# Kernel optimization log

Measured on AMD Instinct MI355X. Metric: run time of the kernel, lower is better.

Reference implementation:

```python
import jax, jax.numpy as jnp
import numpy as np

B, S, D = 1, 4096, 512
H, DK, DV = 8, 64, 64


def setup_inputs() -> dict:
    key = jax.random.key(0)
    ks = jax.random.split(key, 8)
    s = 1.0 / np.sqrt(D)
    return {
        "queries": jax.random.normal(ks[0], (B, S, D), jnp.float32),
        "keys": jax.random.normal(ks[1], (B, S, D), jnp.float32),
        "values": jax.random.normal(ks[2], (B, S, D), jnp.float32),
        # Linear weights stored as [in, out] for x @ W
        "Wq": jax.random.normal(ks[3], (D, H * DK), jnp.float32) * s,
        "Wk": jax.random.normal(ks[4], (D, H * DK), jnp.float32) * s,
        "Wv": jax.random.normal(ks[5], (D, H * DV), jnp.float32) * s,
        "Wo": jax.random.normal(ks[6], (H * DV, D), jnp.float32) * s,
        "bo": jax.random.normal(ks[7], (D,), jnp.float32) * 0.02,
    }


def reference(queries, keys, values, Wq, Wk, Wv, Wo, bo):
    b, qlen = values.shape[0], queries.shape[1]
    q = (queries @ Wq).reshape(b, qlen, H, DK)
    k = (keys @ Wk).reshape(b, keys.shape[1], H, DK)
    v = (values @ Wv).reshape(b, values.shape[1], H, DV)
    scale = DK ** 0.5
    # naive full attention: materialize [b, h, sq, sk] scores
    scores = jnp.einsum("bqhd,bkhd->bhqk", q, k) / scale
    attn = jax.nn.softmax(scores, axis=-1)
    out = jnp.einsum("bhqk,bkhd->bqhd", attn, v).reshape(b, qlen, H * DV)
    out = out @ Wo + bo          # first fc_out
    out = out @ Wo + bo          # second fc_out (module applies it twice when not reversible)
    return out
```

## Files before the change

kernel.cpp:

```cpp
#include <hip/hip_runtime.h>

#define S_LEN  4096
#define DMODEL 512
#define NH     8
#define HD     64

typedef _Float16 f16x8 __attribute__((ext_vector_type(8)));
typedef _Float16 f16x4 __attribute__((ext_vector_type(4)));
typedef float    f32x4 __attribute__((ext_vector_type(4)));

static __device__ __forceinline__ unsigned short f2h(float x) {
  return __builtin_bit_cast(unsigned short, (_Float16)x);
}

__global__ __launch_bounds__(256) void wtrans_kernel(
    const float* __restrict__ w0, const float* __restrict__ w1,
    const float* __restrict__ w2, const float* __restrict__ w3,
    unsigned short* __restrict__ o0, unsigned short* __restrict__ o1,
    unsigned short* __restrict__ o2, unsigned short* __restrict__ o3,
    unsigned short* __restrict__ o3s)
{
  __shared__ unsigned short T[64 * 72];
  const float* W; unsigned short* O;
  switch (blockIdx.z) {
    case 0:  W = w0; O = o0; break;
    case 1:  W = w1; O = o1; break;
    case 2:  W = w2; O = o2; break;
    default: W = w3; O = o3; break;
  }
  const int tid = threadIdx.x;
  const int k0 = blockIdx.x * 64, n0 = blockIdx.y * 64;
  const int c4 = (tid & 15) * 4;
#pragma unroll
  for (int rp = 0; rp < 4; ++rp) {
    int r = rp * 16 + (tid >> 4);
    float4 x = *(const float4*)(W + (k0 + r) * DMODEL + n0 + c4);
    T[(c4 + 0) * 72 + r] = f2h(x.x);
    T[(c4 + 1) * 72 + r] = f2h(x.y);
    T[(c4 + 2) * 72 + r] = f2h(x.z);
    T[(c4 + 3) * 72 + r] = f2h(x.w);
    if (blockIdx.z == 3) {
      f16x4 st;
      st[0] = (_Float16)x.x; st[1] = (_Float16)x.y;
      st[2] = (_Float16)x.z; st[3] = (_Float16)x.w;
      *(f16x4*)&o3s[(k0 + r) * DMODEL + n0 + c4] = st;
    }
  }
  __syncthreads();
#pragma unroll
  for (int it = 0; it < 2; ++it) {
    int i = tid + it * 256;
    int nl = i >> 3, c = i & 7;
    *(f16x8*)&O[(n0 + nl) * DMODEL + k0 + c * 8] = *(const f16x8*)&T[nl * 72 + c * 8];
  }
}

__global__ __launch_bounds__(256) void gemm_kernel(
    const void* __restrict__ A0, const void* __restrict__ A1,
    const void* __restrict__ A2, const void* __restrict__ A3,
    const unsigned short* __restrict__ B0, const unsigned short* __restrict__ B1,
    const unsigned short* __restrict__ B2, const unsigned short* __restrict__ B3,
    void* __restrict__ C0, void* __restrict__ C1,
    void* __restrict__ C2, void* __restrict__ C3,
    const float* __restrict__ bias, unsigned short* __restrict__ vtg,
    const float* __restrict__ wo_f32, const float* __restrict__ bo_in,
    float* __restrict__ bo2_out,
    int a_fp32_mask, int c_fp32_mask)
{
  constexpr int K = DMODEL, N = DMODEL;
  __shared__ unsigned short As[64 * 32];
  __shared__ unsigned short Bs[64 * 32];
  const int z = blockIdx.z;
  if (z == 3 && blockIdx.x >= 8) {
    if (blockIdx.x < 16 && blockIdx.y == 0 && wo_f32) {
      int col = (blockIdx.x - 8) * 64 + (threadIdx.x & 63);
      float s = bo_in[col];
#pragma unroll 8
      for (int j = 0; j < DMODEL; ++j) s = fmaf(bo_in[j], wo_f32[j * DMODEL + col], s);
      bo2_out[col] = s;
    }
    return;
  }
  const void* Av; const unsigned short* Bt; void* Cv;
  switch (z) {
    case 0:  Av = A0; Bt = B0; Cv = C0; break;
    case 1:  Av = A1; Bt = B1; Cv = C1; break;
    case 2:  Av = A2; Bt = B2; Cv = C2; break;
    default: Av = A3; Bt = B3; Cv = C3; break;
  }
  const int a_fp32 = (a_fp32_mask >> z) & 1;
  const int c_fp32 = (c_fp32_mask >> z) & 1;
  const int tid  = threadIdx.x;
  const int lane = tid & 63;
  const int wid  = tid >> 6;
  const int quad = lane >> 4, l16 = lane & 15;
  const int m0 = blockIdx.x * 64, n0 = blockIdx.y * 64;
  const int wm = (wid >> 1) * 32, wn = (wid & 1) * 32;
  const int r  = tid >> 2, ck = (tid & 3) * 8;
  f32x4 acc[2][2] = {};

  for (int k0 = 0; k0 < K; k0 += 32) {
    __syncthreads();
    if (a_fp32) {
      const float* p = (const float*)Av + (m0 + r) * K + k0 + ck;
      float4 x = *(const float4*)p;
      float4 y = *(const float4*)(p + 4);
      f16x8 av;
      av[0] = (_Float16)x.x; av[1] = (_Float16)x.y;
      av[2] = (_Float16)x.z; av[3] = (_Float16)x.w;
      av[4] = (_Float16)y.x; av[5] = (_Float16)y.y;
      av[6] = (_Float16)y.z; av[7] = (_Float16)y.w;
      *(f16x8*)&As[r * 32 + ck] = av;
    } else {
      *(f16x8*)&As[r * 32 + ck] =
          *(const f16x8*)((const unsigned short*)Av + (m0 + r) * K + k0 + ck);
    }
    *(f16x8*)&Bs[r * 32 + ck] = *(const f16x8*)(Bt + (n0 + r) * K + k0 + ck);
    __syncthreads();

    f16x8 a0 = *(const f16x8*)&As[(wm + l16) * 32 + quad * 8];
    f16x8 a1 = *(const f16x8*)&As[(wm + 16 + l16) * 32 + quad * 8];
    f16x8 b0 = *(const f16x8*)&Bs[(wn + l16) * 32 + quad * 8];
    f16x8 b1 = *(const f16x8*)&Bs[(wn + 16 + l16) * 32 + quad * 8];
    acc[0][0] = __builtin_amdgcn_mfma_f32_16x16x32_f16(a0, b0, acc[0][0], 0, 0, 0);
    acc[0][1] = __builtin_amdgcn_mfma_f32_16x16x32_f16(a0, b1, acc[0][1], 0, 0, 0);
    acc[1][0] = __builtin_amdgcn_mfma_f32_16x16x32_f16(a1, b0, acc[1][0], 0, 0, 0);
    acc[1][1] = __builtin_amdgcn_mfma_f32_16x16x32_f16(a1, b1, acc[1][1], 0, 0, 0);
  }

  const int do_vt = (vtg != nullptr) && (z == 2);
#pragma unroll
  for (int mt = 0; mt < 2; ++mt)
#pragma unroll
    for (int nt = 0; nt < 2; ++nt) {
      int col = n0 + wn + nt * 16 + l16;
      float bv = bias ? bias[col] : 0.f;
#pragma unroll
      for (int g = 0; g < 4; ++g) {
        int row = m0 + wm + mt * 16 + quad * 4 + g;
        float val = acc[mt][nt][g] + bv;
        if (do_vt)        vtg[col * S_LEN + row] = f2h(val);
        else if (c_fp32)  ((float*)Cv)[row * N + col] = val;
        else              ((unsigned short*)Cv)[row * N + col] = f2h(val);
      }
    }
}

__global__ __launch_bounds__(256) void attn_kernel(
    const unsigned short* __restrict__ Qb, const unsigned short* __restrict__ Kb,
    const unsigned short* __restrict__ VtG, unsigned short* __restrict__ Ob)
{
  __shared__ unsigned short Ks[2][64 * 72];
  __shared__ unsigned short Vt[2][64 * 72];
  __shared__ _Float16 Osc[2][64][32];
  __shared__ float    Msc[2][2][16];
  __shared__ float    Lsc[2][2][16];

  const int tid  = threadIdx.x;
  const int lane = tid & 63;
  const int wid  = tid >> 6;
  const int qp   = wid & 1;
  const int kh   = wid >> 1;
  const int quad = lane >> 4, l16 = lane & 15;
  const int qb = blockIdx.x, h = blockIdx.y;
  const int hc = h * HD;
  const int qbase = qb * 64 + qp * 32;

  f16x8 bq[2][2];
#pragma unroll
  for (int s = 0; s < 2; ++s) {
    int qrow = qbase + s * 16 + l16;
    bq[s][0] = *(const f16x8*)(Qb + qrow * DMODEL + hc + quad * 8);
    bq[s][1] = *(const f16x8*)(Qb + qrow * DMODEL + hc + 32 + quad * 8);
  }

  f32x4 o[2][4] = {};
  float m_run[2] = {-1e30f, -1e30f}, l_run[2] = {0.f, 0.f};

  f16x8 kreg[4], vreg[4];
#pragma unroll
  for (int it = 0; it < 4; ++it) {
    int s = it * 256 + tid;
    int khs = s >> 9, n = (s >> 3) & 63, c = s & 7;
    kreg[it] = *(const f16x8*)(Kb + (khs * 2048 + n) * DMODEL + hc + c * 8);
    vreg[it] = *(const f16x8*)(VtG + (hc + n) * S_LEN + khs * 2048 + c * 8);
  }

  for (int kbi = 0; kbi < 32; ++kbi) {
    __syncthreads();
#pragma unroll
    for (int it = 0; it < 4; ++it) {
      int s = it * 256 + tid;
      int khs = s >> 9, n = (s >> 3) & 63, c = s & 7;
      *(f16x8*)&Ks[khs][n * 72 + c * 8] = kreg[it];
      *(f16x8*)&Vt[khs][n * 72 + c * 8] = vreg[it];
    }
    __syncthreads();

    if (kbi + 1 < 32) {
      int kb1 = (kbi + 1) * 64;
#pragma unroll
      for (int it = 0; it < 4; ++it) {
        int s = it * 256 + tid;
        int khs = s >> 9, n = (s >> 3) & 63, c = s & 7;
        kreg[it] = *(const f16x8*)(Kb + (khs * 2048 + kb1 + n) * DMODEL + hc + c * 8);
        vreg[it] = *(const f16x8*)(VtG + (hc + n) * S_LEN + khs * 2048 + kb1 + c * 8);
      }
    }

    f32x4 sT[2][4];
#pragma unroll
    for (int kt = 0; kt < 4; ++kt) {
      f16x8 ak0 = *(const f16x8*)&Ks[kh][(kt * 16 + l16) * 72 + quad * 8];
      f16x8 ak1 = *(const f16x8*)&Ks[kh][(kt * 16 + l16) * 72 + 32 + quad * 8];
#pragma unroll
      for (int s = 0; s < 2; ++s) {
        f32x4 a = {};
        a = __builtin_amdgcn_mfma_f32_16x16x32_f16(ak0, bq[s][0], a, 0, 0, 0);
        a = __builtin_amdgcn_mfma_f32_16x16x32_f16(ak1, bq[s][1], a, 0, 0, 0);
        sT[s][kt] = a;
      }
    }

    f16x4 pa[2][4];
#pragma unroll
    for (int s = 0; s < 2; ++s) {
      float vmax = -1e30f;
#pragma unroll
      for (int kt = 0; kt < 4; ++kt)
#pragma unroll
        for (int g = 0; g < 4; ++g) vmax = fmaxf(vmax, sT[s][kt][g]);
      vmax = fmaxf(vmax, __shfl_xor(vmax, 16));
      vmax = fmaxf(vmax, __shfl_xor(vmax, 32));
      const float mn = fmaxf(m_run[s], vmax);
      const float alpha = __expf((m_run[s] - mn) * 0.125f);
      m_run[s] = mn;

      float rs = 0.f;
#pragma unroll
      for (int kt = 0; kt < 4; ++kt)
#pragma unroll
        for (int g = 0; g < 4; ++g) {
          float p = __expf((sT[s][kt][g] - mn) * 0.125f);
          rs += p;
          pa[s][kt][g] = (_Float16)p;
        }
      rs += __shfl_xor(rs, 16);
      rs += __shfl_xor(rs, 32);
      l_run[s] = l_run[s] * alpha + rs;

      float ag[4];
#pragma unroll
      for (int g = 0; g < 4; ++g) ag[g] = __shfl(alpha, quad * 4 + g);
#pragma unroll
      for (int nt = 0; nt < 4; ++nt)
#pragma unroll
        for (int g = 0; g < 4; ++g) o[s][nt][g] *= ag[g];
    }

#pragma unroll
    for (int nt = 0; nt < 4; ++nt)
#pragma unroll
      for (int kt = 0; kt < 4; ++kt) {
        f16x4 bv = *(const f16x4*)&Vt[kh][(nt * 16 + l16) * 72 + kt * 16 + quad * 4];
#pragma unroll
        for (int s = 0; s < 2; ++s)
          o[s][nt] = __builtin_amdgcn_mfma_f32_16x16x16f16(pa[s][kt], bv, o[s][nt], 0, 0, 0);
      }
  }

  __syncthreads();
  if (kh == 1) {
#pragma unroll
    for (int s = 0; s < 2; ++s) {
      if (quad == 0) { Msc[qp][s][l16] = m_run[s]; Lsc[qp][s][l16] = l_run[s]; }
#pragma unroll
      for (int nt = 0; nt < 4; ++nt)
#pragma unroll
        for (int g = 0; g < 4; ++g)
          Osc[qp][lane][s * 16 + nt * 4 + g] = (_Float16)o[s][nt][g];
    }
  }
  __syncthreads();
  if (kh == 0) {
#pragma unroll
    for (int s = 0; s < 2; ++s) {
      const float m1 = Msc[qp][s][l16];
      const float l1 = Lsc[qp][s][l16];
      const float m  = fmaxf(m_run[s], m1);
      const float a0 = __expf((m_run[s] - m) * 0.125f);
      const float a1 = __expf((m1 - m) * 0.125f);
      const float rl = 1.f / (l_run[s] * a0 + l1 * a1);
      float a0g[4], a1g[4], rlg[4];
#pragma unroll
      for (int g = 0; g < 4; ++g) {
        a0g[g] = __shfl(a0, quad * 4 + g);
        a1g[g] = __shfl(a1, quad * 4 + g);
        rlg[g] = __shfl(rl, quad * 4 + g);
      }
#pragma unroll
      for (int g = 0; g < 4; ++g) {
        int row = qbase + s * 16 + quad * 4 + g;
#pragma unroll
        for (int nt = 0; nt < 4; ++nt) {
          float om = o[s][nt][g] * a0g[g] + (float)Osc[qp][lane][s * 16 + nt * 4 + g] * a1g[g];
          Ob[row * DMODEL + hc + nt * 16 + l16] = f2h(om * rlg[g]);
        }
      }
    }
  }
}

extern "C" void kernel_launch(void* const* d_in, const int* in_sizes, int n_in,
                              void* d_out, int out_size, void* d_ws, size_t ws_size,
                              hipStream_t stream) {
  const float* q  = (const float*)d_in[0];
  const float* k  = (const float*)d_in[1];
  const float* v  = (const float*)d_in[2];
  const float* Wq = (const float*)d_in[3];
  const float* Wk = (const float*)d_in[4];
  const float* Wv = (const float*)d_in[5];
  const float* Wo = (const float*)d_in[6];
  const float* bo = (const float*)d_in[7];

  unsigned short* ws   = (unsigned short*)d_ws;
  unsigned short* Wqt  = ws;
  unsigned short* Wkt  = Wqt  + 262144;
  unsigned short* Wvt  = Wkt  + 262144;
  unsigned short* Wot  = Wvt  + 262144;
  unsigned short* Wof  = Wot  + 262144;
  unsigned short* Wo2t = Wof  + 262144;
  unsigned short* Qb   = Wo2t + 262144;
  unsigned short* Kb   = Qb   + 2097152;
  unsigned short* VtG  = Kb   + 2097152;
  unsigned short* Ab   = VtG  + 2097152;
  float*          bo2  = (float*)(Ab + 2097152);

  wtrans_kernel<<<dim3(8, 8, 4), 256, 0, stream>>>(
      Wq, Wk, Wv, Wo, Wqt, Wkt, Wvt, Wot, Wof);

  gemm_kernel<<<dim3(64, 8, 4), 256, 0, stream>>>(
      q, k, v, Wot, Wqt, Wkt, Wvt, Wof, Qb, Kb, nullptr, Wo2t,
      nullptr, VtG, Wo, bo, bo2, 0x7, 0x0);

  attn_kernel<<<dim3(64, 8), 256, 0, stream>>>(Qb, Kb, VtG, Ab);

  gemm_kernel<<<dim3(64, 8, 1), 256, 0, stream>>>(
      Ab, nullptr, nullptr, nullptr, Wo2t, nullptr, nullptr, nullptr,
      d_out, nullptr, nullptr, nullptr, bo2, nullptr,
      nullptr, nullptr, nullptr, 0x0, 0x1);
}
```

Before: 199.0 us.

## Split attention KV into four wave-groups, swizzle V tile, skip unneeded rescales

```diff
diff --git a/kernel.cpp b/kernel.cpp
--- a/kernel.cpp
+++ b/kernel.cpp
@@ -146,15 +146,14 @@
     }
 }
 
-__global__ __launch_bounds__(256) void attn_kernel(
+__global__ __launch_bounds__(512, 4) void attn_kernel(
     const unsigned short* __restrict__ Qb, const unsigned short* __restrict__ Kb,
     const unsigned short* __restrict__ VtG, unsigned short* __restrict__ Ob)
 {
-  __shared__ unsigned short Ks[2][64 * 72];
-  __shared__ unsigned short Vt[2][64 * 72];
-  __shared__ _Float16 Osc[2][64][32];
-  __shared__ float    Msc[2][2][16];
-  __shared__ float    Lsc[2][2][16];
+  __shared__ unsigned short Ks[4][64 * 72];
+  __shared__ unsigned short Vt[4 * 64 * 64];
+  __shared__ float Msc[3][2][2][16];
+  __shared__ float Lsc[3][2][2][16];
 
   const int tid  = threadIdx.x;
   const int lane = tid & 63;
@@ -180,31 +179,36 @@
   f16x8 kreg[4], vreg[4];
 #pragma unroll
   for (int it = 0; it < 4; ++it) {
-    int s = it * 256 + tid;
-    int khs = s >> 9, n = (s >> 3) & 63, c = s & 7;
-    kreg[it] = *(const f16x8*)(Kb + (khs * 2048 + n) * DMODEL + hc + c * 8);
-    vreg[it] = *(const f16x8*)(VtG + (hc + n) * S_LEN + khs * 2048 + c * 8);
-  }
-
-  for (int kbi = 0; kbi < 32; ++kbi) {
+    int s = it * 512 + tid;
+    int sub = s >> 9, n = (s >> 3) & 63, c = s & 7;
+    kreg[it] = *(const f16x8*)(Kb + (sub * 1024 + n) * DMODEL + hc + c * 8);
+    vreg[it] = *(const f16x8*)(VtG + (hc + n) * S_LEN + sub * 1024 + c * 8);
+  }
+
+  for (int kbi = 0; kbi < 16; ++kbi) {
     __syncthreads();
 #pragma unroll
     for (int it = 0; it < 4; ++it) {
-      int s = it * 256 + tid;
-      int khs = s >> 9, n = (s >> 3) & 63, c = s & 7;
-      *(f16x8*)&Ks[khs][n * 72 + c * 8] = kreg[it];
-      *(f16x8*)&Vt[khs][n * 72 + c * 8] = vreg[it];
+      int s = it * 512 + tid;
+      int sub = s >> 9, n = (s >> 3) & 63, c = s & 7;
+      *(f16x8*)&Ks[sub][n * 72 + c * 8] = kreg[it];
+      int vbase = (sub * 64 + n) * 16;
+      int n15 = n & 15;
+      f16x4 lo = __builtin_shufflevector(vreg[it], vreg[it], 0, 1, 2, 3);
+      f16x4 hi = __builtin_shufflevector(vreg[it], vreg[it], 4, 5, 6, 7);
+      *(f16x4*)&Vt[(vbase + ((2 * c) ^ n15)) * 4]     = lo;
+      *(f16x4*)&Vt[(vbase + ((2 * c + 1) ^ n15)) * 4] = hi;
     }
     __syncthreads();
 
-    if (kbi + 1 < 32) {
+    if (kbi + 1 < 16) {
       int kb1 = (kbi + 1) * 64;
 #pragma unroll
       for (int it = 0; it < 4; ++it) {
-        int s = it * 256 + tid;
-        int khs = s >> 9, n = (s >> 3) & 63, c = s & 7;
-        kreg[it] = *(const f16x8*)(Kb + (khs * 2048 + kb1 + n) * DMODEL + hc + c * 8);
-        vreg[it] = *(const f16x8*)(VtG + (hc + n) * S_LEN + khs * 2048 + kb1 + c * 8);
+        int s = it * 512 + tid;
+        int sub = s >> 9, n = (s >> 3) & 63, c = s & 7;
+        kreg[it] = *(const f16x8*)(Kb + (sub * 1024 + kb1 + n) * DMODEL + hc + c * 8);
+        vreg[it] = *(const f16x8*)(VtG + (hc + n) * S_LEN + sub * 1024 + kb1 + c * 8);
       }
     }
 
@@ -232,78 +236,108 @@
         for (int g = 0; g < 4; ++g) vmax = fmaxf(vmax, sT[s][kt][g]);
       vmax = fmaxf(vmax, __shfl_xor(vmax, 16));
       vmax = fmaxf(vmax, __shfl_xor(vmax, 32));
-      const float mn = fmaxf(m_run[s], vmax);
-      const float alpha = __expf((m_run[s] - mn) * 0.125f);
-      m_run[s] = mn;
-
-      float rs = 0.f;
-#pragma unroll
-      for (int kt = 0; kt < 4; ++kt)
-#pragma unroll
-        for (int g = 0; g < 4; ++g) {
-          float p = __expf((sT[s][kt][g] - mn) * 0.125f);
-          rs += p;
-          pa[s][kt][g] = (_Float16)p;
-        }
-      rs += __shfl_xor(rs, 16);
-      rs += __shfl_xor(rs, 32);
-      l_run[s] = l_run[s] * alpha + rs;
-
-      float ag[4];
-#pragma unroll
-      for (int g = 0; g < 4; ++g) ag[g] = __shfl(alpha, quad * 4 + g);
-#pragma unroll
-      for (int nt = 0; nt < 4; ++nt)
-#pragma unroll
-        for (int g = 0; g < 4; ++g) o[s][nt][g] *= ag[g];
-    }
-
-#pragma unroll
-    for (int nt = 0; nt < 4; ++nt)
+
+      if (__all(vmax <= m_run[s] + 8.0f)) {
+        const float mn = m_run[s];
+        float rs = 0.f;
+#pragma unroll
+        for (int kt = 0; kt < 4; ++kt)
+#pragma unroll
+          for (int g = 0; g < 4; ++g) {
+            float p = __expf((sT[s][kt][g] - mn) * 0.125f);
+            rs += p;
+            pa[s][kt][g] = (_Float16)p;
+          }
+        rs += __shfl_xor(rs, 16);
+        rs += __shfl_xor(rs, 32);
+        l_run[s] += rs;
+      } else {
+        const float mn = fmaxf(m_run[s], vmax);
+        const float alpha = __expf((m_run[s] - mn) * 0.125f);
+        m_run[s] = mn;
+
+        float rs = 0.f;
+#pragma unroll
+        for (int kt = 0; kt < 4; ++kt)
+#pragma unroll
+          for (int g = 0; g < 4; ++g) {
+            float p = __expf((sT[s][kt][g] - mn) * 0.125f);
+            rs += p;
+            pa[s][kt][g] = (_Float16)p;
+          }
+        rs += __shfl_xor(rs, 16);
+        rs += __shfl_xor(rs, 32);
+        l_run[s] = l_run[s] * alpha + rs;
+
+        float ag[4];
+#pragma unroll
+        for (int g = 0; g < 4; ++g) ag[g] = __shfl(alpha, quad * 4 + g);
+#pragma unroll
+        for (int nt = 0; nt < 4; ++nt)
+#pragma unroll
+          for (int g = 0; g < 4; ++g) o[s][nt][g] *= ag[g];
+      }
+    }
+
+#pragma unroll
+    for (int nt = 0; nt < 4; ++nt) {
+      int dbase = (kh * 64 + nt * 16 + l16) * 16;
 #pragma unroll
       for (int kt = 0; kt < 4; ++kt) {
-        f16x4 bv = *(const f16x4*)&Vt[kh][(nt * 16 + l16) * 72 + kt * 16 + quad * 4];
+        f16x4 bv = *(const f16x4*)&Vt[(dbase + ((kt * 4 + quad) ^ l16)) * 4];
 #pragma unroll
         for (int s = 0; s < 2; ++s)
           o[s][nt] = __builtin_amdgcn_mfma_f32_16x16x16f16(pa[s][kt], bv, o[s][nt], 0, 0, 0);
       }
+    }
   }
 
   __syncthreads();
-  if (kh == 1) {
+  _Float16* Osc = (_Float16*)&Ks[0][0];
+  if (kh > 0) {
+    const int ki = kh - 1;
 #pragma unroll
     for (int s = 0; s < 2; ++s) {
-      if (quad == 0) { Msc[qp][s][l16] = m_run[s]; Lsc[qp][s][l16] = l_run[s]; }
+      if (quad == 0) { Msc[ki][qp][s][l16] = m_run[s]; Lsc[ki][qp][s][l16] = l_run[s]; }
 #pragma unroll
       for (int nt = 0; nt < 4; ++nt)
 #pragma unroll
         for (int g = 0; g < 4; ++g)
-          Osc[qp][lane][s * 16 + nt * 4 + g] = (_Float16)o[s][nt][g];
+          Osc[((ki * 2 + qp) * 64 + lane) * 36 + s * 16 + nt * 4 + g] = (_Float16)o[s][nt][g];
     }
   }
   __syncthreads();
   if (kh == 0) {
 #pragma unroll
     for (int s = 0; s < 2; ++s) {
-      const float m1 = Msc[qp][s][l16];
-      const float l1 = Lsc[qp][s][l16];
-      const float m  = fmaxf(m_run[s], m1);
+      const float m1 = Msc[0][qp][s][l16], m2 = Msc[1][qp][s][l16], m3 = Msc[2][qp][s][l16];
+      const float l1 = Lsc[0][qp][s][l16], l2 = Lsc[1][qp][s][l16], l3 = Lsc[2][qp][s][l16];
+      const float m  = fmaxf(fmaxf(m_run[s], m1), fmaxf(m2, m3));
       const float a0 = __expf((m_run[s] - m) * 0.125f);
       const float a1 = __expf((m1 - m) * 0.125f);
-      const float rl = 1.f / (l_run[s] * a0 + l1 * a1);
-      float a0g[4], a1g[4], rlg[4];
+      const float a2 = __expf((m2 - m) * 0.125f);
+      const float a3 = __expf((m3 - m) * 0.125f);
+      const float rl = 1.f / (l_run[s] * a0 + l1 * a1 + l2 * a2 + l3 * a3);
+      float a0g[4], a1g[4], a2g[4], a3g[4], rlg[4];
 #pragma unroll
       for (int g = 0; g < 4; ++g) {
-        a0g[g] = __shfl(a0, quad * 4 + g);
-        a1g[g] = __shfl(a1, quad * 4 + g);
-        rlg[g] = __shfl(rl, quad * 4 + g);
+        int src = quad * 4 + g;
+        a0g[g] = __shfl(a0, src);
+        a1g[g] = __shfl(a1, src);
+        a2g[g] = __shfl(a2, src);
+        a3g[g] = __shfl(a3, src);
+        rlg[g] = __shfl(rl, src);
       }
 #pragma unroll
       for (int g = 0; g < 4; ++g) {
         int row = qbase + s * 16 + quad * 4 + g;
 #pragma unroll
         for (int nt = 0; nt < 4; ++nt) {
-          float om = o[s][nt][g] * a0g[g] + (float)Osc[qp][lane][s * 16 + nt * 4 + g] * a1g[g];
+          int idx = s * 16 + nt * 4 + g;
+          float om = o[s][nt][g] * a0g[g]
+                   + (float)Osc[((0 + qp) * 64 + lane) * 36 + idx] * a1g[g]
+                   + (float)Osc[((2 + qp) * 64 + lane) * 36 + idx] * a2g[g]
+                   + (float)Osc[((4 + qp) * 64 + lane) * 36 + idx] * a3g[g];
           Ob[row * DMODEL + hc + nt * 16 + l16] = f2h(om * rlg[g]);
         }
       }
@@ -343,7 +377,7 @@
       q, k, v, Wot, Wqt, Wkt, Wvt, Wof, Qb, Kb, nullptr, Wo2t,
       nullptr, VtG, Wo, bo, bo2, 0x7, 0x0);
 
-  attn_kernel<<<dim3(64, 8), 256, 0, stream>>>(Qb, Kb, VtG, Ab);
+  attn_kernel<<<dim3(64, 8), 512, 0, stream>>>(Qb, Kb, VtG, Ab);
 
   gemm_kernel<<<dim3(64, 8, 1), 256, 0, stream>>>(
       Ab, nullptr, nullptr, nullptr, Wo2t, nullptr, nullptr, nullptr,
```

New measurement: 390.6 us. 96.3% more time.

## Split attention keys across two grid slices with a merge kernel

Applied to the files above, without the earlier changes.

```diff
diff --git a/kernel.cpp b/kernel.cpp
--- a/kernel.cpp
+++ b/kernel.cpp
@@ -148,13 +148,14 @@
 
 __global__ __launch_bounds__(256) void attn_kernel(
     const unsigned short* __restrict__ Qb, const unsigned short* __restrict__ Kb,
-    const unsigned short* __restrict__ VtG, unsigned short* __restrict__ Ob)
+    const unsigned short* __restrict__ VtG,
+    float* __restrict__ P0, unsigned short* __restrict__ P1,
+    float* __restrict__ mp, float* __restrict__ lp)
 {
   __shared__ unsigned short Ks[2][64 * 72];
-  __shared__ unsigned short Vt[2][64 * 72];
-  __shared__ _Float16 Osc[2][64][32];
-  __shared__ float    Msc[2][2][16];
-  __shared__ float    Lsc[2][2][16];
+  __shared__ unsigned short Vt[2 * 64 * 64];
+  __shared__ float Msc[2][2][16];
+  __shared__ float Lsc[2][2][16];
 
   const int tid  = threadIdx.x;
   const int lane = tid & 63;
@@ -162,9 +163,10 @@
   const int qp   = wid & 1;
   const int kh   = wid >> 1;
   const int quad = lane >> 4, l16 = lane & 15;
-  const int qb = blockIdx.x, h = blockIdx.y;
+  const int qb = blockIdx.x, h = blockIdx.y, z = blockIdx.z;
   const int hc = h * HD;
   const int qbase = qb * 64 + qp * 32;
+  const int kz = z * 2048;
 
   f16x8 bq[2][2];
 #pragma unroll
@@ -182,29 +184,34 @@
   for (int it = 0; it < 4; ++it) {
     int s = it * 256 + tid;
     int khs = s >> 9, n = (s >> 3) & 63, c = s & 7;
-    kreg[it] = *(const f16x8*)(Kb + (khs * 2048 + n) * DMODEL + hc + c * 8);
-    vreg[it] = *(const f16x8*)(VtG + (hc + n) * S_LEN + khs * 2048 + c * 8);
-  }
-
-  for (int kbi = 0; kbi < 32; ++kbi) {
+    kreg[it] = *(const f16x8*)(Kb + (kz + khs * 1024 + n) * DMODEL + hc + c * 8);
+    vreg[it] = *(const f16x8*)(VtG + (hc + n) * S_LEN + kz + khs * 1024 + c * 8);
+  }
+
+  for (int kbi = 0; kbi < 16; ++kbi) {
     __syncthreads();
 #pragma unroll
     for (int it = 0; it < 4; ++it) {
       int s = it * 256 + tid;
       int khs = s >> 9, n = (s >> 3) & 63, c = s & 7;
       *(f16x8*)&Ks[khs][n * 72 + c * 8] = kreg[it];
-      *(f16x8*)&Vt[khs][n * 72 + c * 8] = vreg[it];
+      int vbase = (khs * 64 + n) * 16;
+      int n15 = n & 15;
+      f16x4 lo = __builtin_shufflevector(vreg[it], vreg[it], 0, 1, 2, 3);
+      f16x4 hi = __builtin_shufflevector(vreg[it], vreg[it], 4, 5, 6, 7);
+      *(f16x4*)&Vt[(vbase + ((2 * c) ^ n15)) * 4]     = lo;
+      *(f16x4*)&Vt[(vbase + ((2 * c + 1) ^ n15)) * 4] = hi;
     }
     __syncthreads();
 
-    if (kbi + 1 < 32) {
+    if (kbi + 1 < 16) {
       int kb1 = (kbi + 1) * 64;
 #pragma unroll
       for (int it = 0; it < 4; ++it) {
         int s = it * 256 + tid;
         int khs = s >> 9, n = (s >> 3) & 63, c = s & 7;
-        kreg[it] = *(const f16x8*)(Kb + (khs * 2048 + kb1 + n) * DMODEL + hc + c * 8);
-        vreg[it] = *(const f16x8*)(VtG + (hc + n) * S_LEN + khs * 2048 + kb1 + c * 8);
+        kreg[it] = *(const f16x8*)(Kb + (kz + khs * 1024 + kb1 + n) * DMODEL + hc + c * 8);
+        vreg[it] = *(const f16x8*)(VtG + (hc + n) * S_LEN + kz + khs * 1024 + kb1 + c * 8);
       }
     }
 
@@ -232,44 +239,64 @@
         for (int g = 0; g < 4; ++g) vmax = fmaxf(vmax, sT[s][kt][g]);
       vmax = fmaxf(vmax, __shfl_xor(vmax, 16));
       vmax = fmaxf(vmax, __shfl_xor(vmax, 32));
-      const float mn = fmaxf(m_run[s], vmax);
-      const float alpha = __expf((m_run[s] - mn) * 0.125f);
-      m_run[s] = mn;
-
-      float rs = 0.f;
-#pragma unroll
-      for (int kt = 0; kt < 4; ++kt)
-#pragma unroll
-        for (int g = 0; g < 4; ++g) {
-          float p = __expf((sT[s][kt][g] - mn) * 0.125f);
-          rs += p;
-          pa[s][kt][g] = (_Float16)p;
-        }
-      rs += __shfl_xor(rs, 16);
-      rs += __shfl_xor(rs, 32);
-      l_run[s] = l_run[s] * alpha + rs;
-
-      float ag[4];
-#pragma unroll
-      for (int g = 0; g < 4; ++g) ag[g] = __shfl(alpha, quad * 4 + g);
-#pragma unroll
-      for (int nt = 0; nt < 4; ++nt)
-#pragma unroll
-        for (int g = 0; g < 4; ++g) o[s][nt][g] *= ag[g];
-    }
-
-#pragma unroll
-    for (int nt = 0; nt < 4; ++nt)
+
+      if (__all(vmax <= m_run[s] + 8.0f)) {
+        const float mn = m_run[s];
+        float rs = 0.f;
+#pragma unroll
+        for (int kt = 0; kt < 4; ++kt)
+#pragma unroll
+          for (int g = 0; g < 4; ++g) {
+            float p = __expf((sT[s][kt][g] - mn) * 0.125f);
+            rs += p;
+            pa[s][kt][g] = (_Float16)p;
+          }
+        rs += __shfl_xor(rs, 16);
+        rs += __shfl_xor(rs, 32);
+        l_run[s] += rs;
+      } else {
+        const float mn = fmaxf(m_run[s], vmax);
+        const float alpha = __expf((m_run[s] - mn) * 0.125f);
+        m_run[s] = mn;
+
+        float rs = 0.f;
+#pragma unroll
+        for (int kt = 0; kt < 4; ++kt)
+#pragma unroll
+          for (int g = 0; g < 4; ++g) {
+            float p = __expf((sT[s][kt][g] - mn) * 0.125f);
+            rs += p;
+            pa[s][kt][g] = (_Float16)p;
+          }
+        rs += __shfl_xor(rs, 16);
+        rs += __shfl_xor(rs, 32);
+        l_run[s] = l_run[s] * alpha + rs;
+
+        float ag[4];
+#pragma unroll
+        for (int g = 0; g < 4; ++g) ag[g] = __shfl(alpha, quad * 4 + g);
+#pragma unroll
+        for (int nt = 0; nt < 4; ++nt)
+#pragma unroll
+          for (int g = 0; g < 4; ++g) o[s][nt][g] *= ag[g];
+      }
+    }
+
+#pragma unroll
+    for (int nt = 0; nt < 4; ++nt) {
+      int dbase = (kh * 64 + nt * 16 + l16) * 16;
 #pragma unroll
       for (int kt = 0; kt < 4; ++kt) {
-        f16x4 bv = *(const f16x4*)&Vt[kh][(nt * 16 + l16) * 72 + kt * 16 + quad * 4];
+        f16x4 bv = *(const f16x4*)&Vt[(dbase + ((kt * 4 + quad) ^ l16)) * 4];
 #pragma unroll
         for (int s = 0; s < 2; ++s)
           o[s][nt] = __builtin_amdgcn_mfma_f32_16x16x16f16(pa[s][kt], bv, o[s][nt], 0, 0, 0);
       }
+    }
   }
 
   __syncthreads();
+  _Float16* Osc = (_Float16*)&Ks[0][0];
   if (kh == 1) {
 #pragma unroll
     for (int s = 0; s < 2; ++s) {
@@ -278,7 +305,7 @@
       for (int nt = 0; nt < 4; ++nt)
 #pragma unroll
         for (int g = 0; g < 4; ++g)
-          Osc[qp][lane][s * 16 + nt * 4 + g] = (_Float16)o[s][nt][g];
+          Osc[(qp * 64 + lane) * 32 + s * 16 + nt * 4 + g] = (_Float16)o[s][nt][g];
     }
   }
   __syncthreads();
@@ -290,7 +317,13 @@
       const float m  = fmaxf(m_run[s], m1);
       const float a0 = __expf((m_run[s] - m) * 0.125f);
       const float a1 = __expf((m1 - m) * 0.125f);
-      const float rl = 1.f / (l_run[s] * a0 + l1 * a1);
+      const float lt = l_run[s] * a0 + l1 * a1;
+      const float rl = 1.f / lt;
+      if (quad == 0) {
+        int q = qbase + s * 16 + l16;
+        mp[(z * NH + h) * S_LEN + q] = m;
+        lp[(z * NH + h) * S_LEN + q] = lt;
+      }
       float a0g[4], a1g[4], rlg[4];
 #pragma unroll
       for (int g = 0; g < 4; ++g) {
@@ -303,12 +336,58 @@
         int row = qbase + s * 16 + quad * 4 + g;
 #pragma unroll
         for (int nt = 0; nt < 4; ++nt) {
-          float om = o[s][nt][g] * a0g[g] + (float)Osc[qp][lane][s * 16 + nt * 4 + g] * a1g[g];
-          Ob[row * DMODEL + hc + nt * 16 + l16] = f2h(om * rlg[g]);
+          float om = o[s][nt][g] * a0g[g] + (float)Osc[(qp * 64 + lane) * 32 + s * 16 + nt * 4 + g] * a1g[g];
+          float val = om * rlg[g];
+          if (z == 0) P0[row * DMODEL + hc + nt * 16 + l16] = val;
+          else        P1[row * DMODEL + hc + nt * 16 + l16] = f2h(val);
         }
       }
     }
   }
+}
+
+__global__ __launch_bounds__(256) void merge_kernel(
+    const float* __restrict__ P0, const unsigned short* __restrict__ P1,
+    const float* __restrict__ mp, const float* __restrict__ lp,
+    unsigned short* __restrict__ Ob)
+{
+  const int tid = threadIdx.x;
+  const int qb = blockIdx.x, h = blockIdx.y;
+  const int q = qb * 64 + (tid >> 2), hc = h * HD;
+  const int dq = (tid & 3) * 16;
+  const float m0 = mp[h * S_LEN + q],        l0 = lp[h * S_LEN + q];
+  const float m1 = mp[(NH + h) * S_LEN + q], l1 = lp[(NH + h) * S_LEN + q];
+  const float M  = fmaxf(m0, m1);
+  float w0 = l0 * __expf((m0 - M) * 0.125f);
+  float w1 = l1 * __expf((m1 - M) * 0.125f);
+  const float rw = 1.f / (w0 + w1);
+  w0 *= rw; w1 *= rw;
+  const int base = q * DMODEL + hc + dq;
+  f16x8 p1a = *(const f16x8*)&P1[base];
+  f16x8 p1b = *(const f16x8*)&P1[base + 8];
+  float4 x0 = *(const float4*)&P0[base];
+  float4 x1 = *(const float4*)&P0[base + 4];
+  float4 x2 = *(const float4*)&P0[base + 8];
+  float4 x3 = *(const float4*)&P0[base + 12];
+  f16x8 oa, ob;
+  oa[0] = (_Float16)(w0 * x0.x + w1 * (float)p1a[0]);
+  oa[1] = (_Float16)(w0 * x0.y + w1 * (float)p1a[1]);
+  oa[2] = (_Float16)(w0 * x0.z + w1 * (float)p1a[2]);
+  oa[3] = (_Float16)(w0 * x0.w + w1 * (float)p1a[3]);
+  oa[4] = (_Float16)(w0 * x1.x + w1 * (float)p1a[4]);
+  oa[5] = (_Float16)(w0 * x1.y + w1 * (float)p1a[5]);
+  oa[6] = (_Float16)(w0 * x1.z + w1 * (float)p1a[6]);
+  oa[7] = (_Float16)(w0 * x1.w + w1 * (float)p1a[7]);
+  ob[0] = (_Float16)(w0 * x2.x + w1 * (float)p1b[0]);
+  ob[1] = (_Float16)(w0 * x2.y + w1 * (float)p1b[1]);
+  ob[2] = (_Float16)(w0 * x2.z + w1 * (float)p1b[2]);
+  ob[3] = (_Float16)(w0 * x2.w + w1 * (float)p1b[3]);
+  ob[4] = (_Float16)(w0 * x3.x + w1 * (float)p1b[4]);
+  ob[5] = (_Float16)(w0 * x3.y + w1 * (float)p1b[5]);
+  ob[6] = (_Float16)(w0 * x3.z + w1 * (float)p1b[6]);
+  ob[7] = (_Float16)(w0 * x3.w + w1 * (float)p1b[7]);
+  *(f16x8*)&Ob[base]     = oa;
+  *(f16x8*)&Ob[base + 8] = ob;
 }
 
 extern "C" void kernel_launch(void* const* d_in, const int* in_sizes, int n_in,
@@ -335,6 +414,8 @@
   unsigned short* VtG  = Kb   + 2097152;
   unsigned short* Ab   = VtG  + 2097152;
   float*          bo2  = (float*)(Ab + 2097152);
+  float*          mp   = bo2 + 512;
+  float*          lp   = mp + 65536;
 
   wtrans_kernel<<<dim3(8, 8, 4), 256, 0, stream>>>(
       Wq, Wk, Wv, Wo, Wqt, Wkt, Wvt, Wot, Wof);
@@ -343,7 +424,11 @@
       q, k, v, Wot, Wqt, Wkt, Wvt, Wof, Qb, Kb, nullptr, Wo2t,
       nullptr, VtG, Wo, bo, bo2, 0x7, 0x0);
 
-  attn_kernel<<<dim3(64, 8), 256, 0, stream>>>(Qb, Kb, VtG, Ab);
+  attn_kernel<<<dim3(64, 8, 2), 256, 0, stream>>>(
+      Qb, Kb, VtG, (float*)d_out, Ab, mp, lp);
+
+  merge_kernel<<<dim3(64, 8), 256, 0, stream>>>(
+      (const float*)d_out, Ab, mp, lp, Ab);
 
   gemm_kernel<<<dim3(64, 8, 1), 256, 0, stream>>>(
       Ab, nullptr, nullptr, nullptr, Wo2t, nullptr, nullptr, nullptr,
```

New measurement: 213.6 us. +7.3%, slower.
